# Performance work log

Hardware: AMD Instinct MI355X
Metric: run time of the kernel (lower is better)

Reference implementation:

```python
import jax, jax.numpy as jnp
import numpy as np

DIM = 128
EDGE_COUNT = 128
N_NODES = 128
GRAPH_COUNT = 8
VOCAB = 100000
VEC_DIM = 300


def setup_inputs():
    key = jax.random.key(0)
    ks = jax.random.split(key, 8)
    rng = np.random.default_rng(0)
    data = jnp.asarray(rng.integers(0, VOCAB, size=N_NODES), dtype=jnp.int32)
    types = jnp.zeros((N_NODES,), dtype=jnp.int32)  # single data_type
    edges = jnp.asarray(rng.integers(0, EDGE_COUNT, size=N_NODES), dtype=jnp.int32)
    # parent-offset trees: node i's parent is a node > i, last node is the single root (offset 0)
    g = np.zeros((GRAPH_COUNT, N_NODES), dtype=np.int32)
    for j in range(GRAPH_COUNT):
        for i in range(N_NODES - 1):
            p = int(rng.integers(i + 1, N_NODES))
            g[j, i] = p - i
    graphs = jnp.asarray(g)
    inv_sqrt_d = 1.0 / np.sqrt(DIM)
    inv_sqrt_v = 1.0 / np.sqrt(VEC_DIM)
    return {
        "data": data, "types": types, "graphs": graphs, "edges": edges, "pos": 37,
        "data_vecs": jax.random.normal(ks[0], (VOCAB, VEC_DIM), jnp.float32),
        "data_weights": jax.random.normal(ks[1], (VEC_DIM, DIM), jnp.float32) * inv_sqrt_v,
        "data_biases": jax.random.normal(ks[2], (DIM,), jnp.float32) * 0.1,
        "edge_weights": jax.random.normal(ks[3], (EDGE_COUNT, DIM, DIM), jnp.float32) * inv_sqrt_d,
        "edge_biases": jax.random.normal(ks[4], (EDGE_COUNT, DIM), jnp.float32) * 0.1,
        "score_embedding_weights": jax.random.normal(ks[5], (DIM, 1), jnp.float32) * inv_sqrt_d,
        "score_data_weights": jax.random.normal(ks[6], (DIM, 1), jnp.float32) * inv_sqrt_d,
        "score_bias": jax.random.normal(ks[7], (1, 1), jnp.float32),
    }


def _tree_structure(parents_row):
    # Faithful reproduction of calc_embedding's structure handling (numpy on int constants).
    parents = np.asarray(parents_row).copy()
    n = len(parents)
    roots = [i for i in range(n) if parents[i] == 0]
    for i in range(len(roots) - 1):
        parents[roots[i]] = roots[i + 1]
    root = roots[-1]
    parents[root] = -n
    children = {}
    for i in range(n):
        pp = i + int(parents[i])
        children.setdefault(pp, []).append(i)
    order = []  # DFS preorder from root; reversed gives children-before-parent
    stack = [root]
    while stack:
        node = stack.pop()
        order.append(node)
        stack.extend(children.get(node, []))
    return root, children, order


def _forward(data, types, graphs, edges, pos,
             data_vecs, data_weights, data_biases,
             edge_weights, edge_biases,
             score_embedding_weights, score_data_weights, score_bias):
    data_np = np.asarray(data)
    graphs_np = np.asarray(graphs)
    edges_np = np.asarray(edges).copy()
    E, D, _ = edge_weights.shape
    # data embedding + data score for the queried position
    d_emb = data_vecs[data_np[pos]] @ data_weights + data_biases          # (D,)
    d_score = score_bias[0, 0] + d_emb @ score_data_weights[:, 0]         # scalar
    edges_np[pos] = -1  # unknown edge at pos -> branch over all edge types
    # base embeddings for all nodes at once: (N, D)
    base = data_vecs[data_np] @ data_weights + data_biases

    def transform(child_emb, eid):
        # child_emb: (E, D). eid < 0 -> per-edge-type weights (baddbmm over all E edges)
        if eid < 0:
            return jnp.einsum('ed,edk->ek', child_emb, edge_weights) + edge_biases
        return child_emb @ edge_weights[eid] + edge_biases[eid]

    scores = []
    for j in range(graphs_np.shape[0]):
        root, children, order = _tree_structure(graphs_np[j])
        emb = {}
        for n in reversed(order):  # children before parents
            e = jnp.broadcast_to(base[n], (E, D))
            ch = children.get(n, [])
            for c in ch:
                e = e + transform(emb.pop(c), int(edges_np[c]))
            if ch:
                e = jax.nn.relu(e)  # clamp(min=0) only for internal nodes
            emb[n] = e
        res = transform(emb[root], int(edges_np[root]))  # add_child_embedding(zeros, root_emb, edges[root])
        scores.append(d_score + res @ score_embedding_weights[:, 0])  # (E,)
    return jnp.stack(scores)  # (GRAPH_COUNT, EDGE_COUNT)


def reference(data, types, graphs, edges, pos, data_vecs, data_weights, data_biases,
              edge_weights, edge_biases, score_embedding_weights, score_data_weights, score_bias):
    return _forward(data, types, graphs, edges, pos, data_vecs, data_weights, data_biases,
                    edge_weights, edge_biases, score_embedding_weights, score_data_weights, score_bias)
```

## Files before the change

### kernel.cpp

```cpp
#include <hip/hip_runtime.h>
#include <stdint.h>


#define NND 128
#define DD  128
#define GG  8
#define VD  300
#define CH  4

typedef unsigned int u32;

#define F_RELU (1u<<16)
#define F_POS  (1u<<17)
#define F_PATH (1u<<18)

#define SYNC_LDS() asm volatile("s_waitcnt lgkmcnt(0)\n\ts_barrier" ::: "memory")

__global__ void __launch_bounds__(128) k_base(
        const int* __restrict__ data, const int* __restrict__ posArr,
        const float* __restrict__ vecs, const float* __restrict__ dw,
        const float* __restrict__ db,   const float* __restrict__ sdw,
        const float* __restrict__ sb,
        float* __restrict__ base, float* __restrict__ dscore)
{
    __shared__ __align__(16) float row[VD];
    __shared__ float red[DD];
    int n = blockIdx.x, t = threadIdx.x;
    int id = data[n];
    const float4* vp = (const float4*)(vecs + (size_t)id * VD);
    for (int i = t; i < VD/4; i += 128) ((float4*)row)[i] = vp[i];
    __syncthreads();
    float acc = db[t];
    for (int d = 0; d < VD; ++d)
        acc = fmaf(row[d], dw[d*DD + t], acc);
    base[n*DD + t] = acc;
    if (n == posArr[0]){
        red[t] = acc * sdw[t];
        __syncthreads();
        for (int o = 64; o > 0; o >>= 1){ if (t < o) red[t] += red[t+o]; __syncthreads(); }
        if (t == 0) dscore[0] = sb[0] + red[0];
    }
}

__global__ void __launch_bounds__(256, 1) k_tree(
        const int* __restrict__ graphs, const int* __restrict__ edges,
        const int* __restrict__ posArr, const float* __restrict__ EW,
        const float* __restrict__ EB,   const float* __restrict__ base,
        float* __restrict__ vposG, float* __restrict__ uG, int* __restrict__ meta)
{
    __shared__ __align__(16) float acc[NND-1][DD];
    __shared__ u32 desc[NND];
    int g = blockIdx.x, t = threadIdx.x;

    for (int idx = t; idx < (NND-1)*DD/4; idx += 256)
        ((float4*)acc)[idx] = ((const float4*)(base + DD))[idx];

    int myPar = -1;
    if (t < NND){
        myPar = (t < NND-1) ? (t + graphs[g*NND + t]) : 0;
        desc[t] = (u32)(myPar & 0xFF) | ((u32)edges[t] << 8);
    }
    __syncthreads();
    if (t < NND-1) atomicOr(&desc[myPar], F_RELU);
    if (t == 0){
        int p = posArr[0];
        atomicOr(&desc[p], F_POS);
        int c = desc[p] & 0xFF;
        int s = 0;
        for (;;){
            atomicOr(&desc[c], F_PATH | ((u32)s << 24));
            meta[g*(NND+1) + 1 + s] = c;
            ++s;
            if (c == NND-1) break;
            c = desc[c] & 0xFF;
        }
        meta[g*(NND+1)] = s;
    }
    __syncthreads();

    int l = t & 63, w = t >> 6;
    int k4 = w*8 + (l & 7);
    int d0 = (l >> 3) * 16;
    bool owner = ((l >> 3) == 0);

    auto pfW = [&](int edge, float4 (&wr)[16], float4& ebr){
        const float* Wp = EW + (size_t)edge*(DD*DD) + (size_t)d0*DD + 4*k4;
        #pragma unroll
        for (int d = 0; d < 16; ++d) wr[d] = *(const float4*)&Wp[d*DD];
        ebr = *(const float4*)&EB[(size_t)edge*DD + 4*k4];
    };

    auto stepGo = [&](int i, float4 (&wr)[16], float4& ebr, int iPf){
        u32 dsc = desc[i];
        const float* src = (i == 0) ? base : &acc[i-1][0];
        if (dsc & (F_POS | F_PATH)){
            if (dsc & F_POS){
                if (t < DD){
                    float v = src[t];
                    if (dsc & F_RELU) v = fmaxf(v, 0.f);
                    vposG[g*DD + t] = v;
                }
            } else {
                int slot = (int)(dsc >> 24);
                if (t < DD) uG[((size_t)g*NND + slot)*DD + t] = src[t];
            }
        } else {
            int par = (int)(dsc & 0xFF);
            float ev[16];
            #pragma unroll
            for (int j = 0; j < 4; ++j){
                float4 x = *(const float4*)&src[d0 + 4*j];
                ev[4*j+0]=x.x; ev[4*j+1]=x.y; ev[4*j+2]=x.z; ev[4*j+3]=x.w;
            }
            if (dsc & F_RELU){
                #pragma unroll
                for (int j = 0; j < 16; ++j) ev[j] = fmaxf(ev[j], 0.f);
            }
            float s0=0.f, s1=0.f, s2=0.f, s3=0.f;
            #pragma unroll
            for (int d = 0; d < 16; ++d){
                s0 = fmaf(ev[d], wr[d].x, s0);
                s1 = fmaf(ev[d], wr[d].y, s1);
                s2 = fmaf(ev[d], wr[d].z, s2);
                s3 = fmaf(ev[d], wr[d].w, s3);
            }
            #pragma unroll
            for (int m = 8; m <= 32; m <<= 1){
                s0 += __shfl_xor(s0, m);
                s1 += __shfl_xor(s1, m);
                s2 += __shfl_xor(s2, m);
                s3 += __shfl_xor(s3, m);
            }
            if (owner){
                float4* dst = (float4*)&acc[par-1][4*k4];
                float4 o = *dst;
                o.x += s0 + ebr.x; o.y += s1 + ebr.y;
                o.z += s2 + ebr.z; o.w += s3 + ebr.w;
                *dst = o;
            }
        }
        if (iPf < NND){
            int eN = (int)((desc[iPf] >> 8) & 0xFF);
            pfW(eN, wr, ebr);
        }
        SYNC_LDS();
    };

    float4 wA[16], wB[16], ebA, ebB;
    { int e0 = (int)((desc[0] >> 8) & 0xFF); pfW(e0, wA, ebA); }
    { int e1 = (int)((desc[1] >> 8) & 0xFF); pfW(e1, wB, ebB); }
    for (int ii = 0; ii < NND; ii += 2){
        stepGo(ii,     wA, ebA, ii+2);
        stepGo(ii + 1, wB, ebB, ii+3);
    }
}

__global__ void __launch_bounds__(256, 1) k_chain(
        const int* __restrict__ edges,
        const float* __restrict__ EW, const float* __restrict__ EB,
        const float* __restrict__ SEW,
        const float* __restrict__ vposG, const float* __restrict__ uG,
        const int* __restrict__ meta, const float* __restrict__ dscore,
        float* __restrict__ outp)
{
    __shared__ __align__(16) float Vbuf[2][CH][DD];
    __shared__ float red[CH][4];
    int g = blockIdx.x >> 5, chunk = blockIdx.x & 31;
    int t = threadIdx.x, l = t & 63, w = t >> 6;
    int k4 = w*8 + (l & 7);
    int d0 = (l >> 3) * 16;
    bool owner = ((l >> 3) == 0);
    int eBase = chunk * CH;
    int L = meta[g*(NND+1)];

    float vpf[16];
    #pragma unroll
    for (int j = 0; j < 4; ++j){
        float4 x = *(const float4*)&vposG[g*DD + d0 + 4*j];
        vpf[4*j+0]=x.x; vpf[4*j+1]=x.y; vpf[4*j+2]=x.z; vpf[4*j+3]=x.w;
    }
    float4 u0 = *(const float4*)&uG[(size_t)g*NND*DD + 4*k4];

    #pragma unroll 2
    for (int p = 0; p < CH; ++p){
        int e = eBase + p;
        const float* Wp = EW + (size_t)e*(DD*DD) + (size_t)d0*DD + 4*k4;
        float s0=0.f, s1=0.f, s2=0.f, s3=0.f;
        #pragma unroll
        for (int d = 0; d < 16; ++d){
            float4 wv = *(const float4*)&Wp[d*DD];
            s0 = fmaf(vpf[d], wv.x, s0);
            s1 = fmaf(vpf[d], wv.y, s1);
            s2 = fmaf(vpf[d], wv.z, s2);
            s3 = fmaf(vpf[d], wv.w, s3);
        }
        #pragma unroll
        for (int m = 8; m <= 32; m <<= 1){
            s0 += __shfl_xor(s0, m); s1 += __shfl_xor(s1, m);
            s2 += __shfl_xor(s2, m); s3 += __shfl_xor(s3, m);
        }
        if (owner){
            float4 bb = *(const float4*)&EB[(size_t)e*DD + 4*k4];
            float4 r;
            r.x = fmaxf(u0.x + s0 + bb.x, 0.f);
            r.y = fmaxf(u0.y + s1 + bb.y, 0.f);
            r.z = fmaxf(u0.z + s2 + bb.z, 0.f);
            r.w = fmaxf(u0.w + s3 + bb.w, 0.f);
            *(float4*)&Vbuf[0][p][4*k4] = r;
        }
    }
    __syncthreads();

    int cur = 0;
    for (int s = 1; s < L; ++s){
        int pn = meta[g*(NND+1) + s];
        int ej = edges[pn];
        const float* Wp = EW + (size_t)ej*(DD*DD) + (size_t)d0*DD + 4*k4;
        float4 wr[16];
        #pragma unroll
        for (int d = 0; d < 16; ++d) wr[d] = *(const float4*)&Wp[d*DD];
        float4 us = *(const float4*)&uG[((size_t)g*NND + s)*DD + 4*k4];
        float4 bb = *(const float4*)&EB[(size_t)ej*DD + 4*k4];
        #pragma unroll
        for (int p = 0; p < CH; ++p){
            float ev[16];
            #pragma unroll
            for (int j = 0; j < 4; ++j){
                float4 x = *(const float4*)&Vbuf[cur][p][d0 + 4*j];
                ev[4*j+0]=x.x; ev[4*j+1]=x.y; ev[4*j+2]=x.z; ev[4*j+3]=x.w;
            }
            float s0=0.f, s1=0.f, s2=0.f, s3=0.f;
            #pragma unroll
            for (int d = 0; d < 16; ++d){
                s0 = fmaf(ev[d], wr[d].x, s0);
                s1 = fmaf(ev[d], wr[d].y, s1);
                s2 = fmaf(ev[d], wr[d].z, s2);
                s3 = fmaf(ev[d], wr[d].w, s3);
            }
            #pragma unroll
            for (int m = 8; m <= 32; m <<= 1){
                s0 += __shfl_xor(s0, m); s1 += __shfl_xor(s1, m);
                s2 += __shfl_xor(s2, m); s3 += __shfl_xor(s3, m);
            }
            if (owner){
                float4 r;
                r.x = fmaxf(us.x + s0 + bb.x, 0.f);
                r.y = fmaxf(us.y + s1 + bb.y, 0.f);
                r.z = fmaxf(us.z + s2 + bb.z, 0.f);
                r.w = fmaxf(us.w + s3 + bb.w, 0.f);
                *(float4*)&Vbuf[cur^1][p][4*k4] = r;
            }
        }
        __syncthreads();
        cur ^= 1;
    }

    {
        int rn = meta[g*(NND+1) + L];
        int er = edges[rn];
        const float* Wp = EW + (size_t)er*(DD*DD) + (size_t)d0*DD + 4*k4;
        float4 wr[16];
        #pragma unroll
        for (int d = 0; d < 16; ++d) wr[d] = *(const float4*)&Wp[d*DD];
        float4 bb = *(const float4*)&EB[(size_t)er*DD + 4*k4];
        float4 sw = *(const float4*)&SEW[4*k4];
        #pragma unroll
        for (int p = 0; p < CH; ++p){
            float ev[16];
            #pragma unroll
            for (int j = 0; j < 4; ++j){
                float4 x = *(const float4*)&Vbuf[cur][p][d0 + 4*j];
                ev[4*j+0]=x.x; ev[4*j+1]=x.y; ev[4*j+2]=x.z; ev[4*j+3]=x.w;
            }
            float s0=0.f, s1=0.f, s2=0.f, s3=0.f;
            #pragma unroll
            for (int d = 0; d < 16; ++d){
                s0 = fmaf(ev[d], wr[d].x, s0);
                s1 = fmaf(ev[d], wr[d].y, s1);
                s2 = fmaf(ev[d], wr[d].z, s2);
                s3 = fmaf(ev[d], wr[d].w, s3);
            }
            #pragma unroll
            for (int m = 8; m <= 32; m <<= 1){
                s0 += __shfl_xor(s0, m); s1 += __shfl_xor(s1, m);
                s2 += __shfl_xor(s2, m); s3 += __shfl_xor(s3, m);
            }
            if (owner){
                float part = (s0 + bb.x) * sw.x + (s1 + bb.y) * sw.y
                           + (s2 + bb.z) * sw.z + (s3 + bb.w) * sw.w;
                part += __shfl_xor(part, 1);
                part += __shfl_xor(part, 2);
                part += __shfl_xor(part, 4);
                if (l == 0) red[p][w] = part;
            }
        }
        __syncthreads();
        if (t < CH)
            outp[g*DD + eBase + t] = dscore[0] + red[t][0] + red[t][1] + red[t][2] + red[t][3];
    }
}

extern "C" void kernel_launch(void* const* d_in, const int* in_sizes, int n_in,
                              void* d_out, int out_size, void* d_ws, size_t ws_size,
                              hipStream_t stream)
{
    const int*   data   = (const int*)d_in[0];
    const int*   graphs = (const int*)d_in[2];
    const int*   edges  = (const int*)d_in[3];
    const int*   posArr = (const int*)d_in[4];
    const float* vecs   = (const float*)d_in[5];
    const float* dw     = (const float*)d_in[6];
    const float* db     = (const float*)d_in[7];
    const float* ew     = (const float*)d_in[8];
    const float* eb     = (const float*)d_in[9];
    const float* sew    = (const float*)d_in[10];
    const float* sdw    = (const float*)d_in[11];
    const float* sb     = (const float*)d_in[12];

    char* ws = (char*)d_ws;
    float* base   = (float*)(ws);
    float* vposG  = (float*)(ws + 65536);
    float* uG     = (float*)(ws + 65536 + 4096);
    float* dscore = (float*)(ws + 65536 + 4096 + 524288);
    int*   meta   = (int*)  (ws + 65536 + 4096 + 524288 + 256);

    float* outp = (float*)d_out;

    k_base <<<NND, 128, 0, stream>>>(data, posArr, vecs, dw, db, sdw, sb, base, dscore);
    k_tree <<<GG, 256, 0, stream>>>(graphs, edges, posArr, ew, eb, base, vposG, uG, meta);
    k_chain<<<GG*(DD/CH), 256, 0, stream>>>(edges, ew, eb, sew, vposG, uG, meta, dscore, outp);
}
```

Measured before the change: 348.3 us.

## Process tree nodes level-by-level with per-wave node assignment and LDS atomics

Replaces the strictly sequential node-by-node tree walk (one barrier per node, with prefetched weights in registers) with a height-level schedule. Node heights are computed on one thread, and each round distributes the independent nodes of one height across the four waves. Partial results go to the parent through LDS atomicAdd. This cuts the number of barriers to the tree height and parallelises independent subtrees. In exchange it drops the weight prefetch pipelining, adds a serial single-thread pass to compute heights, and rescans the descriptors every round.

```diff
diff --git a/kernel.cpp b/kernel.cpp
--- a/kernel.cpp
+++ b/kernel.cpp
@@ -10,11 +10,9 @@
 
 typedef unsigned int u32;
 
-#define F_RELU (1u<<16)
-#define F_POS  (1u<<17)
-#define F_PATH (1u<<18)
-
-#define SYNC_LDS() asm volatile("s_waitcnt lgkmcnt(0)\n\ts_barrier" ::: "memory")
+#define F_RELU (1u<<15)
+#define F_POS  (1u<<16)
+#define F_PATH (1u<<17)
 
 __global__ void __launch_bounds__(128) k_base(
         const int* __restrict__ data, const int* __restrict__ posArr,
@@ -48,110 +46,124 @@
         const float* __restrict__ EB,   const float* __restrict__ base,
         float* __restrict__ vposG, float* __restrict__ uG, int* __restrict__ meta)
 {
-    __shared__ __align__(16) float acc[NND-1][DD];
+    __shared__ __align__(16) float accL[NND-1][DD];
     __shared__ u32 desc[NND];
     int g = blockIdx.x, t = threadIdx.x;
+    int l = t & 63, w = t >> 6;
 
     for (int idx = t; idx < (NND-1)*DD/4; idx += 256)
-        ((float4*)acc)[idx] = ((const float4*)(base + DD))[idx];
-
-    int myPar = -1;
+        ((float4*)accL)[idx] = ((const float4*)(base + DD))[idx];
     if (t < NND){
-        myPar = (t < NND-1) ? (t + graphs[g*NND + t]) : 0;
-        desc[t] = (u32)(myPar & 0xFF) | ((u32)edges[t] << 8);
+        int par = (t < NND-1) ? (t + graphs[g*NND + t]) : 0;
+        desc[t] = (u32)par | ((u32)edges[t] << 7);
     }
     __syncthreads();
-    if (t < NND-1) atomicOr(&desc[myPar], F_RELU);
     if (t == 0){
         int p = posArr[0];
-        atomicOr(&desc[p], F_POS);
-        int c = desc[p] & 0xFF;
-        int s = 0;
-        for (;;){
-            atomicOr(&desc[c], F_PATH | ((u32)s << 24));
-            meta[g*(NND+1) + 1 + s] = c;
-            ++s;
-            if (c == NND-1) break;
-            c = desc[c] & 0xFF;
-        }
-        meta[g*(NND+1)] = s;
+        desc[p] |= F_POS;
+        {
+            int c = (int)(desc[p] & 0x7F), s = 0;
+            for (;;){
+                desc[c] |= F_PATH | ((u32)s << 25);
+                meta[g*(NND+1) + 1 + s] = c;
+                ++s;
+                if (c == NND-1) break;
+                c = (int)(desc[c] & 0x7F);
+            }
+            meta[g*(NND+1)] = s;
+        }
+        int mx = 0;
+        for (int i = 0; i < NND-1; ++i){
+            u32 d = desc[i];
+            int pp = (int)(d & 0x7F);
+            desc[pp] |= F_RELU;
+            if (d & (F_POS | F_PATH)) continue;
+            int lv = (int)((d >> 18) & 0x7F);
+            if (lv > mx) mx = lv;
+            u32 dp = desc[pp];
+            int lp = (int)((dp >> 18) & 0x7F);
+            if (lv + 1 > lp)
+                desc[pp] = (dp & ~(0x7Fu << 18)) | ((u32)(lv + 1) << 18);
+        }
+        desc[NND-1] = (desc[NND-1] & ~0x7Fu) | (u32)(mx + 1);
     }
     __syncthreads();
 
-    int l = t & 63, w = t >> 6;
-    int k4 = w*8 + (l & 7);
-    int d0 = (l >> 3) * 16;
-    bool owner = ((l >> 3) == 0);
-
-    auto pfW = [&](int edge, float4 (&wr)[16], float4& ebr){
-        const float* Wp = EW + (size_t)edge*(DD*DD) + (size_t)d0*DD + 4*k4;
-        #pragma unroll
-        for (int d = 0; d < 16; ++d) wr[d] = *(const float4*)&Wp[d*DD];
-        ebr = *(const float4*)&EB[(size_t)edge*DD + 4*k4];
-    };
-
-    auto stepGo = [&](int i, float4 (&wr)[16], float4& ebr, int iPf){
-        u32 dsc = desc[i];
-        const float* src = (i == 0) ? base : &acc[i-1][0];
-        if (dsc & (F_POS | F_PATH)){
-            if (dsc & F_POS){
-                if (t < DD){
-                    float v = src[t];
-                    if (dsc & F_RELU) v = fmaxf(v, 0.f);
-                    vposG[g*DD + t] = v;
+    int nrounds = (int)(desc[NND-1] & 0x7F);
+    int h  = l >> 5;
+    int c0 = 4 * (l & 31);
+    int pos = posArr[0];
+
+    for (int r = 0; r < nrounds; ++r){
+        int m = 0;
+        for (int i = 0; i < NND-1; ++i){
+            u32 d = desc[i];
+            if (d & (F_POS | F_PATH)) continue;
+            if ((int)((d >> 18) & 0x7F) != r) continue;
+            if ((m++ & 3) != w) continue;
+            int par  = (int)(d & 0x7F);
+            int e    = (int)((d >> 7) & 0xFF);
+            bool rl  = (d & F_RELU) != 0;
+            const float* Wp = EW + (size_t)e*(DD*DD) + (size_t)(h*64)*DD + c0;
+            float s0=0.f, s1=0.f, s2=0.f, s3=0.f;
+            if (i == 0){
+                const float* sp = base + h*64;
+                #pragma unroll 4
+                for (int d4 = 0; d4 < 16; ++d4){
+                    float4 av = *(const float4*)&sp[4*d4];
+                    if (rl){ av.x=fmaxf(av.x,0.f); av.y=fmaxf(av.y,0.f);
+                             av.z=fmaxf(av.z,0.f); av.w=fmaxf(av.w,0.f); }
+                    float4 w0 = *(const float4*)&Wp[(4*d4+0)*DD];
+                    float4 w1 = *(const float4*)&Wp[(4*d4+1)*DD];
+                    float4 w2 = *(const float4*)&Wp[(4*d4+2)*DD];
+                    float4 w3 = *(const float4*)&Wp[(4*d4+3)*DD];
+                    s0=fmaf(av.x,w0.x,s0); s1=fmaf(av.x,w0.y,s1); s2=fmaf(av.x,w0.z,s2); s3=fmaf(av.x,w0.w,s3);
+                    s0=fmaf(av.y,w1.x,s0); s1=fmaf(av.y,w1.y,s1); s2=fmaf(av.y,w1.z,s2); s3=fmaf(av.y,w1.w,s3);
+                    s0=fmaf(av.z,w2.x,s0); s1=fmaf(av.z,w2.y,s1); s2=fmaf(av.z,w2.z,s2); s3=fmaf(av.z,w2.w,s3);
+                    s0=fmaf(av.w,w3.x,s0); s1=fmaf(av.w,w3.y,s1); s2=fmaf(av.w,w3.z,s2); s3=fmaf(av.w,w3.w,s3);
                 }
             } else {
-                int slot = (int)(dsc >> 24);
-                if (t < DD) uG[((size_t)g*NND + slot)*DD + t] = src[t];
-            }
-        } else {
-            int par = (int)(dsc & 0xFF);
-            float ev[16];
-            #pragma unroll
-            for (int j = 0; j < 4; ++j){
-                float4 x = *(const float4*)&src[d0 + 4*j];
-                ev[4*j+0]=x.x; ev[4*j+1]=x.y; ev[4*j+2]=x.z; ev[4*j+3]=x.w;
-            }
-            if (dsc & F_RELU){
-                #pragma unroll
-                for (int j = 0; j < 16; ++j) ev[j] = fmaxf(ev[j], 0.f);
-            }
-            float s0=0.f, s1=0.f, s2=0.f, s3=0.f;
-            #pragma unroll
-            for (int d = 0; d < 16; ++d){
-                s0 = fmaf(ev[d], wr[d].x, s0);
-                s1 = fmaf(ev[d], wr[d].y, s1);
-                s2 = fmaf(ev[d], wr[d].z, s2);
-                s3 = fmaf(ev[d], wr[d].w, s3);
-            }
-            #pragma unroll
-            for (int m = 8; m <= 32; m <<= 1){
-                s0 += __shfl_xor(s0, m);
-                s1 += __shfl_xor(s1, m);
-                s2 += __shfl_xor(s2, m);
-                s3 += __shfl_xor(s3, m);
-            }
-            if (owner){
-                float4* dst = (float4*)&acc[par-1][4*k4];
-                float4 o = *dst;
-                o.x += s0 + ebr.x; o.y += s1 + ebr.y;
-                o.z += s2 + ebr.z; o.w += s3 + ebr.w;
-                *dst = o;
-            }
-        }
-        if (iPf < NND){
-            int eN = (int)((desc[iPf] >> 8) & 0xFF);
-            pfW(eN, wr, ebr);
-        }
-        SYNC_LDS();
-    };
-
-    float4 wA[16], wB[16], ebA, ebB;
-    { int e0 = (int)((desc[0] >> 8) & 0xFF); pfW(e0, wA, ebA); }
-    { int e1 = (int)((desc[1] >> 8) & 0xFF); pfW(e1, wB, ebB); }
-    for (int ii = 0; ii < NND; ii += 2){
-        stepGo(ii,     wA, ebA, ii+2);
-        stepGo(ii + 1, wB, ebB, ii+3);
+                const float* sp = &accL[i-1][h*64];
+                #pragma unroll 4
+                for (int d4 = 0; d4 < 16; ++d4){
+                    float4 av = *(const float4*)&sp[4*d4];
+                    if (rl){ av.x=fmaxf(av.x,0.f); av.y=fmaxf(av.y,0.f);
+                             av.z=fmaxf(av.z,0.f); av.w=fmaxf(av.w,0.f); }
+                    float4 w0 = *(const float4*)&Wp[(4*d4+0)*DD];
+                    float4 w1 = *(const float4*)&Wp[(4*d4+1)*DD];
+                    float4 w2 = *(const float4*)&Wp[(4*d4+2)*DD];
+                    float4 w3 = *(const float4*)&Wp[(4*d4+3)*DD];
+                    s0=fmaf(av.x,w0.x,s0); s1=fmaf(av.x,w0.y,s1); s2=fmaf(av.x,w0.z,s2); s3=fmaf(av.x,w0.w,s3);
+                    s0=fmaf(av.y,w1.x,s0); s1=fmaf(av.y,w1.y,s1); s2=fmaf(av.y,w1.z,s2); s3=fmaf(av.y,w1.w,s3);
+                    s0=fmaf(av.z,w2.x,s0); s1=fmaf(av.z,w2.y,s1); s2=fmaf(av.z,w2.z,s2); s3=fmaf(av.z,w2.w,s3);
+                    s0=fmaf(av.w,w3.x,s0); s1=fmaf(av.w,w3.y,s1); s2=fmaf(av.w,w3.z,s2); s3=fmaf(av.w,w3.w,s3);
+                }
+            }
+            s0 += __shfl_xor(s0, 32); s1 += __shfl_xor(s1, 32);
+            s2 += __shfl_xor(s2, 32); s3 += __shfl_xor(s3, 32);
+            if (l < 32){
+                float4 bb = *(const float4*)&EB[(size_t)e*DD + c0];
+                atomicAdd(&accL[par-1][c0+0], s0 + bb.x);
+                atomicAdd(&accL[par-1][c0+1], s1 + bb.y);
+                atomicAdd(&accL[par-1][c0+2], s2 + bb.z);
+                atomicAdd(&accL[par-1][c0+3], s3 + bb.w);
+            }
+        }
+        __syncthreads();
+    }
+
+    if (t < DD){
+        u32 dp = desc[pos];
+        float v = (pos == 0) ? base[t] : accL[pos-1][t];
+        if (dp & F_RELU) v = fmaxf(v, 0.f);
+        vposG[g*DD + t] = v;
+    }
+    for (int i = 1; i < NND; ++i){
+        u32 d = desc[i];
+        if ((d & F_PATH) && t < DD){
+            int s = (int)(d >> 25);
+            uG[((size_t)g*NND + s)*DD + t] = accL[i-1][t];
+        }
     }
 }
 
```

Result: slower. 458.5 us (+31.6%).

## Compact tree schedule, widen k_tree to 512 threads, vectorize base projection

Applied to the files above, without the earlier changes.

The tree kernel now builds a compacted list of only the nodes that need a child transform, skipping the pos node and path nodes instead of stepping through all 128 with branches. It uses 512 threads, so each thread holds 8 weight rows instead of 16, and the wave reduction widens accordingly. Path and pos outputs are written once at the end. The base projection loop reads the LDS row as float4. The serial single-thread schedule build adds setup latency, and the extra shuffle stage adds a little reduction cost per step.

```diff
diff --git a/kernel.cpp b/kernel.cpp
--- a/kernel.cpp
+++ b/kernel.cpp
@@ -9,10 +9,6 @@
 #define CH  4
 
 typedef unsigned int u32;
-
-#define F_RELU (1u<<16)
-#define F_POS  (1u<<17)
-#define F_PATH (1u<<18)
 
 #define SYNC_LDS() asm volatile("s_waitcnt lgkmcnt(0)\n\ts_barrier" ::: "memory")
 
@@ -31,8 +27,14 @@
     for (int i = t; i < VD/4; i += 128) ((float4*)row)[i] = vp[i];
     __syncthreads();
     float acc = db[t];
-    for (int d = 0; d < VD; ++d)
-        acc = fmaf(row[d], dw[d*DD + t], acc);
+    #pragma unroll 5
+    for (int d4 = 0; d4 < VD/4; ++d4){
+        float4 r = *(const float4*)&row[4*d4];
+        acc = fmaf(r.x, dw[(4*d4+0)*DD + t], acc);
+        acc = fmaf(r.y, dw[(4*d4+1)*DD + t], acc);
+        acc = fmaf(r.z, dw[(4*d4+2)*DD + t], acc);
+        acc = fmaf(r.w, dw[(4*d4+3)*DD + t], acc);
+    }
     base[n*DD + t] = acc;
     if (n == posArr[0]){
         red[t] = acc * sdw[t];
@@ -42,116 +44,118 @@
     }
 }
 
-__global__ void __launch_bounds__(256, 1) k_tree(
+__global__ void __launch_bounds__(512, 2) k_tree(
         const int* __restrict__ graphs, const int* __restrict__ edges,
         const int* __restrict__ posArr, const float* __restrict__ EW,
         const float* __restrict__ EB,   const float* __restrict__ base,
         float* __restrict__ vposG, float* __restrict__ uG, int* __restrict__ meta)
 {
-    __shared__ __align__(16) float acc[NND-1][DD];
-    __shared__ u32 desc[NND];
+    __shared__ __align__(16) float accL[NND+1][DD];
+    __shared__ u32 nfo[NND];
+    __shared__ u32 sinfo[NND];
+    __shared__ int pathL[NND];
+    __shared__ int ctl[2];
     int g = blockIdx.x, t = threadIdx.x;
-
-    for (int idx = t; idx < (NND-1)*DD/4; idx += 256)
-        ((float4*)acc)[idx] = ((const float4*)(base + DD))[idx];
-
-    int myPar = -1;
-    if (t < NND){
-        myPar = (t < NND-1) ? (t + graphs[g*NND + t]) : 0;
-        desc[t] = (u32)(myPar & 0xFF) | ((u32)edges[t] << 8);
-    }
-    __syncthreads();
-    if (t < NND-1) atomicOr(&desc[myPar], F_RELU);
+    int l = t & 63, w = t >> 6;
+
+    for (int idx = t; idx < NND*DD/4; idx += 512)
+        ((float4*)accL)[idx] = ((const float4*)base)[idx];
+    if (t < NND)
+        nfo[t] = (t < NND-1) ? (u32)(t + graphs[g*NND + t]) : 0xFFu;
+    __syncthreads();
+    if (t < NND-1) atomicOr(&nfo[nfo[t] & 0xFFu], 0x100u);
+    __syncthreads();
+    int pos = posArr[0];
     if (t == 0){
-        int p = posArr[0];
-        atomicOr(&desc[p], F_POS);
-        int c = desc[p] & 0xFF;
-        int s = 0;
+        int c = (int)(nfo[pos] & 0xFFu), s = 0;
         for (;;){
-            atomicOr(&desc[c], F_PATH | ((u32)s << 24));
-            meta[g*(NND+1) + 1 + s] = c;
+            nfo[c] |= 0x200u;
+            pathL[s] = c;
             ++s;
             if (c == NND-1) break;
-            c = desc[c] & 0xFF;
-        }
+            c = (int)(nfo[c] & 0xFFu);
+        }
+        ctl[0] = s;
         meta[g*(NND+1)] = s;
-    }
-    __syncthreads();
-
-    int l = t & 63, w = t >> 6;
-    int k4 = w*8 + (l & 7);
-    int d0 = (l >> 3) * 16;
-    bool owner = ((l >> 3) == 0);
-
-    auto pfW = [&](int edge, float4 (&wr)[16], float4& ebr){
-        const float* Wp = EW + (size_t)edge*(DD*DD) + (size_t)d0*DD + 4*k4;
-        #pragma unroll
-        for (int d = 0; d < 16; ++d) wr[d] = *(const float4*)&Wp[d*DD];
-        ebr = *(const float4*)&EB[(size_t)edge*DD + 4*k4];
+        for (int q = 0; q < s; ++q) meta[g*(NND+1) + 1 + q] = pathL[q];
+        int m = 0;
+        for (int i = 0; i < NND-1; ++i){
+            u32 nf = nfo[i];
+            if (i == pos || (nf & 0x200u)) continue;
+            sinfo[m++] = (u32)i | ((nf & 0xFFu) << 8)
+                       | ((nf & 0x100u) ? 0x10000u : 0u)
+                       | ((u32)edges[i] << 17);
+        }
+        if (m & 1) sinfo[m++] = (128u << 8);
+        ctl[1] = m;
+    }
+    __syncthreads();
+    int nst = ctl[1];
+
+    int cbase = 16*w + 4*(l & 3);
+    int dg = l >> 2;
+
+    auto PF = [&](u32 si, float4 (&W)[8], float4& bb){
+        int e = (int)((si >> 17) & 0x7Fu);
+        const float* Wp = EW + (size_t)e*(DD*DD) + (size_t)(8*dg)*DD + cbase;
+        #pragma unroll
+        for (int k = 0; k < 8; ++k) W[k] = *(const float4*)(Wp + k*DD);
+        bb = *(const float4*)&EB[(size_t)e*DD + cbase];
     };
-
-    auto stepGo = [&](int i, float4 (&wr)[16], float4& ebr, int iPf){
-        u32 dsc = desc[i];
-        const float* src = (i == 0) ? base : &acc[i-1][0];
-        if (dsc & (F_POS | F_PATH)){
-            if (dsc & F_POS){
-                if (t < DD){
-                    float v = src[t];
-                    if (dsc & F_RELU) v = fmaxf(v, 0.f);
-                    vposG[g*DD + t] = v;
-                }
-            } else {
-                int slot = (int)(dsc >> 24);
-                if (t < DD) uG[((size_t)g*NND + slot)*DD + t] = src[t];
-            }
-        } else {
-            int par = (int)(dsc & 0xFF);
-            float ev[16];
-            #pragma unroll
-            for (int j = 0; j < 4; ++j){
-                float4 x = *(const float4*)&src[d0 + 4*j];
-                ev[4*j+0]=x.x; ev[4*j+1]=x.y; ev[4*j+2]=x.z; ev[4*j+3]=x.w;
-            }
-            if (dsc & F_RELU){
-                #pragma unroll
-                for (int j = 0; j < 16; ++j) ev[j] = fmaxf(ev[j], 0.f);
-            }
-            float s0=0.f, s1=0.f, s2=0.f, s3=0.f;
-            #pragma unroll
-            for (int d = 0; d < 16; ++d){
-                s0 = fmaf(ev[d], wr[d].x, s0);
-                s1 = fmaf(ev[d], wr[d].y, s1);
-                s2 = fmaf(ev[d], wr[d].z, s2);
-                s3 = fmaf(ev[d], wr[d].w, s3);
-            }
-            #pragma unroll
-            for (int m = 8; m <= 32; m <<= 1){
-                s0 += __shfl_xor(s0, m);
-                s1 += __shfl_xor(s1, m);
-                s2 += __shfl_xor(s2, m);
-                s3 += __shfl_xor(s3, m);
-            }
-            if (owner){
-                float4* dst = (float4*)&acc[par-1][4*k4];
-                float4 o = *dst;
-                o.x += s0 + ebr.x; o.y += s1 + ebr.y;
-                o.z += s2 + ebr.z; o.w += s3 + ebr.w;
-                *dst = o;
-            }
-        }
-        if (iPf < NND){
-            int eN = (int)((desc[iPf] >> 8) & 0xFF);
-            pfW(eN, wr, ebr);
-        }
+    auto STEP = [&](u32 si, const float4 (&W)[8], const float4& bb){
+        int n   = (int)(si & 0xFFu);
+        int par = (int)((si >> 8) & 0xFFu);
+        float4 sa = *(const float4*)&accL[n][8*dg];
+        float4 sbv = *(const float4*)&accL[n][8*dg + 4];
+        if (si & 0x10000u){
+            sa.x=fmaxf(sa.x,0.f); sa.y=fmaxf(sa.y,0.f);
+            sa.z=fmaxf(sa.z,0.f); sa.w=fmaxf(sa.w,0.f);
+            sbv.x=fmaxf(sbv.x,0.f); sbv.y=fmaxf(sbv.y,0.f);
+            sbv.z=fmaxf(sbv.z,0.f); sbv.w=fmaxf(sbv.w,0.f);
+        }
+        float s0, s1, s2, s3;
+        s0 = sa.x*W[0].x; s1 = sa.x*W[0].y; s2 = sa.x*W[0].z; s3 = sa.x*W[0].w;
+        s0 = fmaf(sa.y,W[1].x,s0); s1 = fmaf(sa.y,W[1].y,s1); s2 = fmaf(sa.y,W[1].z,s2); s3 = fmaf(sa.y,W[1].w,s3);
+        s0 = fmaf(sa.z,W[2].x,s0); s1 = fmaf(sa.z,W[2].y,s1); s2 = fmaf(sa.z,W[2].z,s2); s3 = fmaf(sa.z,W[2].w,s3);
+        s0 = fmaf(sa.w,W[3].x,s0); s1 = fmaf(sa.w,W[3].y,s1); s2 = fmaf(sa.w,W[3].z,s2); s3 = fmaf(sa.w,W[3].w,s3);
+        s0 = fmaf(sbv.x,W[4].x,s0); s1 = fmaf(sbv.x,W[4].y,s1); s2 = fmaf(sbv.x,W[4].z,s2); s3 = fmaf(sbv.x,W[4].w,s3);
+        s0 = fmaf(sbv.y,W[5].x,s0); s1 = fmaf(sbv.y,W[5].y,s1); s2 = fmaf(sbv.y,W[5].z,s2); s3 = fmaf(sbv.y,W[5].w,s3);
+        s0 = fmaf(sbv.z,W[6].x,s0); s1 = fmaf(sbv.z,W[6].y,s1); s2 = fmaf(sbv.z,W[6].z,s2); s3 = fmaf(sbv.z,W[6].w,s3);
+        s0 = fmaf(sbv.w,W[7].x,s0); s1 = fmaf(sbv.w,W[7].y,s1); s2 = fmaf(sbv.w,W[7].z,s2); s3 = fmaf(sbv.w,W[7].w,s3);
+        #pragma unroll
+        for (int mm = 4; mm <= 32; mm <<= 1){
+            s0 += __shfl_xor(s0, mm); s1 += __shfl_xor(s1, mm);
+            s2 += __shfl_xor(s2, mm); s3 += __shfl_xor(s3, mm);
+        }
+        if (l < 4){
+            float4* dst = (float4*)&accL[par][cbase];
+            float4 o = *dst;
+            o.x += s0 + bb.x; o.y += s1 + bb.y;
+            o.z += s2 + bb.z; o.w += s3 + bb.w;
+            *dst = o;
+        }
+    };
+
+    u32 siA = sinfo[0], siB = sinfo[1];
+    float4 WA[8], WB[8], bbA, bbB;
+    PF(siA, WA, bbA);
+    PF(siB, WB, bbB);
+    for (int j = 0; j < nst; j += 2){
+        STEP(siA, WA, bbA);
+        if (j + 2 < nst){ siA = sinfo[j+2]; PF(siA, WA, bbA); }
         SYNC_LDS();
-    };
-
-    float4 wA[16], wB[16], ebA, ebB;
-    { int e0 = (int)((desc[0] >> 8) & 0xFF); pfW(e0, wA, ebA); }
-    { int e1 = (int)((desc[1] >> 8) & 0xFF); pfW(e1, wB, ebB); }
-    for (int ii = 0; ii < NND; ii += 2){
-        stepGo(ii,     wA, ebA, ii+2);
-        stepGo(ii + 1, wB, ebB, ii+3);
+        STEP(siB, WB, bbB);
+        if (j + 3 < nst){ siB = sinfo[j+3]; PF(siB, WB, bbB); }
+        SYNC_LDS();
+    }
+
+    if (t < DD){
+        float v = accL[pos][t];
+        if (nfo[pos] & 0x100u) v = fmaxf(v, 0.f);
+        vposG[g*DD + t] = v;
+        int L = ctl[0];
+        for (int s = 0; s < L; ++s)
+            uG[((size_t)g*NND + s)*DD + t] = accL[pathL[s]][t];
     }
 }
 
@@ -327,6 +331,6 @@
     float* outp = (float*)d_out;
 
     k_base <<<NND, 128, 0, stream>>>(data, posArr, vecs, dw, db, sdw, sb, base, dscore);
-    k_tree <<<GG, 256, 0, stream>>>(graphs, edges, posArr, ew, eb, base, vposG, uG, meta);
+    k_tree <<<GG, 512, 0, stream>>>(graphs, edges, posArr, ew, eb, base, vposG, uG, meta);
     k_chain<<<GG*(DD/CH), 256, 0, stream>>>(edges, ew, eb, sew, vposG, uG, meta, dscore, outp);
 }
```

After: 378.6 us. +8.7%, slower.
